# Kernel optimization log

Measured on AMD Instinct MI355X. Metric: run time of the kernel, lower is better.

The kernel has to match this reference:

```python
import jax, jax.numpy as jnp
import numpy as np

B, T, S, V, D, H = 32, 50, 40, 32000, 512, 1024


def setup_inputs() -> dict:
    key = jax.random.key(0)
    ks = jax.random.split(key, 14)
    s_ih = 1.0 / np.sqrt(H)
    return {
        "zh_gruths": jax.random.randint(ks[0], (B, T), 0, V),
        "encoder_hs": jax.random.normal(ks[1], (B, S, H), jnp.float32),
        "encoder_h_n": jax.random.normal(ks[2], (1, B, H), jnp.float32) * 0.1,
        "encoder_c_n": jax.random.normal(ks[3], (1, B, H), jnp.float32) * 0.1,
        "entext_len": jax.random.randint(ks[4], (B,), 1, S + 1),
        "teacher_forcing_ratio": 1,
        "emb": jax.random.normal(ks[5], (V, D), jnp.float32) * 0.02,
        "W_ih": jax.random.normal(ks[6], (4 * H, D), jnp.float32) * s_ih,
        "W_hh": jax.random.normal(ks[7], (4 * H, H), jnp.float32) * s_ih,
        "b_ih": jax.random.normal(ks[8], (4 * H,), jnp.float32) * s_ih,
        "b_hh": jax.random.normal(ks[9], (4 * H,), jnp.float32) * s_ih,
        "W_ht": jax.random.normal(ks[10], (H, 2 * H), jnp.float32) * (1.0 / np.sqrt(2 * H)),
        "b_ht": jnp.zeros((H,), jnp.float32),
        "W_voc": jax.random.normal(ks[11], (V, H), jnp.float32) * s_ih,
        "b_voc": jnp.zeros((V,), jnp.float32),
    }


def reference(zh_gruths, encoder_hs, encoder_h_n, encoder_c_n, entext_len,
              teacher_forcing_ratio, emb, W_ih, W_hh, b_ih, b_hh,
              W_ht, b_ht, W_voc, b_voc):
    # teacher_forcing_ratio == 1 -> always teacher forcing (deterministic branch)
    xs = jnp.swapaxes(emb[zh_gruths], 0, 1)  # [T, B, D]
    hx0, cx0 = encoder_h_n[0], encoder_c_n[0]  # [B, H]

    def step(carry, xt):
        hx, cx = carry
        gates = xt @ W_ih.T + b_ih + hx @ W_hh.T + b_hh  # [B, 4H]
        i, f, g, o = jnp.split(gates, 4, axis=-1)  # torch gate order i,f,g,o
        i, f, o = jax.nn.sigmoid(i), jax.nn.sigmoid(f), jax.nn.sigmoid(o)
        cx = f * cx + i * jnp.tanh(g)
        hx = o * jnp.tanh(cx)
        # dot attention over encoder states
        scores = jnp.einsum('bsh,bh->bs', encoder_hs, hx)
        attn = jax.nn.softmax(scores, axis=-1)
        ctx = jnp.einsum('bs,bsh->bh', attn, encoder_hs)
        hx_atten = jnp.tanh(jnp.concatenate([ctx, hx], axis=-1) @ W_ht.T + b_ht)
        logits_t = hx_atten @ W_voc.T + b_voc  # [B, V]
        return (hx, cx), logits_t

    _, logits = jax.lax.scan(step, (hx0, cx0), xs)  # [T, B, V]
    logits = jnp.swapaxes(logits, 0, 1)  # [B, T, V]
    predicts = jnp.argmax(logits, axis=-1)  # [B, T]
    return logits, predicts
```

## Files before the change

kernel.cpp:

```cpp
#include <hip/hip_runtime.h>
#include <math.h>

typedef short bf16x8 __attribute__((ext_vector_type(8)));
typedef float f32x4 __attribute__((ext_vector_type(4)));
typedef float f32x2 __attribute__((ext_vector_type(2)));
typedef unsigned int uint;
typedef uint u32x4 __attribute__((ext_vector_type(4)));
typedef unsigned long long ull;
typedef unsigned short ushort;

#define Bz 32
#define Tz 50
#define Sz 40
#define Vz 32000
#define Dz 512
#define Hz 1024
#define Mz 1600
#define Mp 1664

__device__ __forceinline__ float bf2f(ushort h) {
    uint u = ((uint)h) << 16;
    return __builtin_bit_cast(float, u);
}
__device__ __forceinline__ void splitf(float f, ushort& hi, ushort& lo) {
    uint u = __builtin_bit_cast(uint, f);
    hi = (ushort)(u >> 16);
    float rem = f - __builtin_bit_cast(float, u & 0xFFFF0000u);
    lo = (ushort)(__builtin_bit_cast(uint, rem) >> 16);
}
__device__ __forceinline__ float sigf(float x) { return 1.f / (1.f + expf(-x)); }

__device__ __forceinline__ uint ld_sc1(const uint* p) {
    uint v;
    asm volatile("global_load_dword %0, %1, off sc0 sc1\n\ts_waitcnt vmcnt(0)"
                 : "=&v"(v) : "v"(p) : "memory");
    return v;
}
__device__ __forceinline__ void st_sc1(uint* p, uint v) {
    asm volatile("global_store_dword %0, %1, off sc0 sc1" :: "v"(p), "v"(v) : "memory");
}

__global__ __launch_bounds__(256) void k_pre(ushort* hxA_hi, ushort* hxA_lo, float* cx,
                                             ushort* AH_hi, ushort* AH_lo, uint* flags,
                                             const float* h0, const float* c0) {
    int gid = blockIdx.x * 256 + threadIdx.x;
    if (gid < 32768) {
        float v = h0[gid];
        ushort hi, lo;
        splitf(v, hi, lo);
        hxA_hi[gid] = hi;
        hxA_lo[gid] = lo;
    } else if (gid < 65536) {
        cx[gid - 32768] = c0[gid - 32768];
    } else if (gid < 196608) {
        int g = gid - 65536;
        AH_hi[(long)Mz * 2048 + g] = 0;
        AH_lo[(long)Mz * 2048 + g] = 0;
    } else if (gid < 196608 + 2048) {
        st_sc1(&flags[gid - 196608], 0u);
    }
}

__global__ __launch_bounds__(256) void k_wsplit(const float* __restrict__ src,
                                                ushort* __restrict__ hi, ushort* __restrict__ lo,
                                                int n4) {
    int stride = gridDim.x * 256;
    for (int i = blockIdx.x * 256 + threadIdx.x; i < n4; i += stride) {
        float4 f = *(const float4*)(src + (long)i * 4);
        float vv[4] = {f.x, f.y, f.z, f.w};
        ushort h[4], l[4];
#pragma unroll
        for (int e = 0; e < 4; ++e) splitf(vv[e], h[e], l[e]);
        uint2 hp, lp;
        hp.x = (uint)h[0] | ((uint)h[1] << 16);
        hp.y = (uint)h[2] | ((uint)h[3] << 16);
        lp.x = (uint)l[0] | ((uint)l[1] << 16);
        lp.y = (uint)l[2] | ((uint)l[3] << 16);
        *(uint2*)(hi + (long)i * 4) = hp;
        *(uint2*)(lo + (long)i * 4) = lp;
    }
}

__global__ __launch_bounds__(256, 1) void k_xgemm(const float* __restrict__ emb,
                                                  const int* __restrict__ tok,
                                                  const float* __restrict__ Wih,
                                                  const float* __restrict__ bih,
                                                  const float* __restrict__ bhh,
                                                  float* __restrict__ gx) {
    __shared__ ushort sAh[128][40];
    __shared__ ushort sAl[128][40];
    __shared__ ushort sBh[128][40];
    __shared__ ushort sBl[128][40];
    int bid = blockIdx.x;
    int mt = bid >> 5, nt = bid & 31;
    int tid = threadIdx.x;
    int row = tid >> 1, half = tid & 1;
    int wv = tid >> 6, lane = tid & 63;
    int wr = wv >> 1, wc = wv & 1;
    int m0 = wr * 64, n0 = wc * 64;
    int r16 = lane & 15, kg = lane >> 4, k0 = kg * 8;

    f32x4 acc[4][4];
#pragma unroll
    for (int i = 0; i < 4; i++)
#pragma unroll
        for (int j = 0; j < 4; j++) acc[i][j] = (f32x4){0.f, 0.f, 0.f, 0.f};

    int r = mt * 128 + row;
    int tk = (r < Mz) ? tok[r] : 0;
    const float* arow = emb + (long)tk * Dz;
    const float* brow = Wih + (long)(nt * 128 + row) * Dz;

    for (int kb = 0; kb < Dz; kb += 32) {
        {
            ushort hh[16], ll[16];
#pragma unroll
            for (int q = 0; q < 16; q += 4) {
                float4 w4 = (r < Mz) ? *(const float4*)(arow + kb + half * 16 + q)
                                     : (float4){0.f, 0.f, 0.f, 0.f};
                float vv[4] = {w4.x, w4.y, w4.z, w4.w};
#pragma unroll
                for (int e = 0; e < 4; ++e) splitf(vv[e], hh[q + e], ll[q + e]);
            }
            *(uint4*)&sAh[row][half * 16]     = *(uint4*)&hh[0];
            *(uint4*)&sAh[row][half * 16 + 8] = *(uint4*)&hh[8];
            *(uint4*)&sAl[row][half * 16]     = *(uint4*)&ll[0];
            *(uint4*)&sAl[row][half * 16 + 8] = *(uint4*)&ll[8];
        }
        {
            ushort hh[16], ll[16];
#pragma unroll
            for (int q = 0; q < 16; q += 4) {
                float4 w4 = *(const float4*)(brow + kb + half * 16 + q);
                float vv[4] = {w4.x, w4.y, w4.z, w4.w};
#pragma unroll
                for (int e = 0; e < 4; ++e) splitf(vv[e], hh[q + e], ll[q + e]);
            }
            *(uint4*)&sBh[row][half * 16]     = *(uint4*)&hh[0];
            *(uint4*)&sBh[row][half * 16 + 8] = *(uint4*)&hh[8];
            *(uint4*)&sBl[row][half * 16]     = *(uint4*)&ll[0];
            *(uint4*)&sBl[row][half * 16 + 8] = *(uint4*)&ll[8];
        }
        __syncthreads();
        bf16x8 af[4], alf[4], bhf[4], blf[4];
#pragma unroll
        for (int i = 0; i < 4; ++i) {
            af[i]  = *(const bf16x8*)&sAh[m0 + i * 16 + r16][k0];
            alf[i] = *(const bf16x8*)&sAl[m0 + i * 16 + r16][k0];
            bhf[i] = *(const bf16x8*)&sBh[n0 + i * 16 + r16][k0];
            blf[i] = *(const bf16x8*)&sBl[n0 + i * 16 + r16][k0];
        }
#pragma unroll
        for (int i = 0; i < 4; ++i)
#pragma unroll
            for (int jn = 0; jn < 4; ++jn) {
                acc[i][jn] = __builtin_amdgcn_mfma_f32_16x16x32_bf16(af[i],  bhf[jn], acc[i][jn], 0, 0, 0);
                acc[i][jn] = __builtin_amdgcn_mfma_f32_16x16x32_bf16(af[i],  blf[jn], acc[i][jn], 0, 0, 0);
                acc[i][jn] = __builtin_amdgcn_mfma_f32_16x16x32_bf16(alf[i], bhf[jn], acc[i][jn], 0, 0, 0);
            }
        __syncthreads();
    }
#pragma unroll
    for (int i = 0; i < 4; ++i) {
        int gr0 = mt * 128 + m0 + i * 16 + kg * 4;
#pragma unroll
        for (int reg = 0; reg < 4; ++reg) {
            int gr = gr0 + reg;
            if (gr >= Mz) continue;
#pragma unroll
            for (int jn = 0; jn < 4; ++jn) {
                int gc = nt * 128 + n0 + jn * 16 + r16;
                gx[(long)gr * 4096 + gc] = acc[i][jn][reg] + bih[gc] + bhh[gc];
            }
        }
    }
}

__global__ __launch_bounds__(512, 1) void k_recfused5(
    const float* __restrict__ gx,
    const ushort* __restrict__ Whi, const ushort* __restrict__ Wlo,
    ushort* __restrict__ hxA_hi, ushort* __restrict__ hxA_lo,
    float* __restrict__ hxh, float* __restrict__ cx,
    const float* __restrict__ enc,
    ushort* __restrict__ AH_hi, ushort* __restrict__ AH_lo,
    uint* flags,
    const float* __restrict__ Wvoc, ushort* __restrict__ Wvh, ushort* __restrict__ Wvl,
    int do_wsplit) {
    __shared__ u32x4 stg4[8192];
    __shared__ float hxs[Hz];
    __shared__ float sc[64];
    __shared__ float aw[64];
    int wid = blockIdx.x, tid = threadIdx.x;

    if (wid >= 96) {
        if (do_wsplit) {
            int n4 = Vz * Hz / 4;
            int stride = 160 * 512;
            for (int i = (wid - 96) * 512 + tid; i < n4; i += stride) {
                float4 f = *(const float4*)(Wvoc + (long)i * 4);
                float vv[4] = {f.x, f.y, f.z, f.w};
                ushort h[4], l[4];
#pragma unroll
                for (int e = 0; e < 4; ++e) splitf(vv[e], h[e], l[e]);
                uint2 hp, lp;
                hp.x = (uint)h[0] | ((uint)h[1] << 16);
                hp.y = (uint)h[2] | ((uint)h[3] << 16);
                lp.x = (uint)l[0] | ((uint)l[1] << 16);
                lp.y = (uint)l[2] | ((uint)l[3] << 16);
                *(uint2*)(Wvh + (long)i * 4) = hp;
                *(uint2*)(Wvl + (long)i * 4) = lp;
            }
        }
        return;
    }

    int lane = tid & 63, kh = tid >> 6;

    for (int t = 0; t <= Tz; ++t) {
        if (wid < 64) {
            if (t < Tz) {
                int w = wid;
                int p = t & 1, q = p ^ 1;
                {
                    bool done = false;
                    while (!done) {
                        uint f = 0xFFFFFFFFu;
                        if (lane < 8) f = ld_sc1(&flags[(kh * 8 + lane) * 16]);
                        done = (bool)__all(f >= (uint)t);
                        if (!done) __builtin_amdgcn_s_sleep(1);
                    }
                }
                int kslot = kh * 16 + (lane & 15);
                int rowb = (lane >> 4) * 8;
                const ushort* ph = hxA_hi + p * 32768 + (long)rowb * 1024 + kslot * 8;
                const ushort* pl = hxA_lo + p * 32768 + (long)rowb * 1024 + kslot * 8;
                {
                    u32x4 d0, d1, d2, d3, d4, d5, d6, d7;
                    asm volatile(
                        "global_load_dwordx4 %0, %8, off sc0 sc1\n\t"
                        "global_load_dwordx4 %1, %9, off sc0 sc1\n\t"
                        "global_load_dwordx4 %2, %10, off sc0 sc1\n\t"
                        "global_load_dwordx4 %3, %11, off sc0 sc1\n\t"
                        "global_load_dwordx4 %4, %12, off sc0 sc1\n\t"
                        "global_load_dwordx4 %5, %13, off sc0 sc1\n\t"
                        "global_load_dwordx4 %6, %14, off sc0 sc1\n\t"
                        "global_load_dwordx4 %7, %15, off sc0 sc1\n\t"
                        "s_waitcnt vmcnt(0)"
                        : "=&v"(d0), "=&v"(d1), "=&v"(d2), "=&v"(d3),
                          "=&v"(d4), "=&v"(d5), "=&v"(d6), "=&v"(d7)
                        : "v"(ph), "v"(ph + 1024), "v"(ph + 2048), "v"(ph + 3072),
                          "v"(ph + 4096), "v"(ph + 5120), "v"(ph + 6144), "v"(ph + 7168)
                        : "memory");
                    int li = kslot * 32;
                    stg4[li + ((rowb + 0 + kslot) & 31)] = d0;
                    stg4[li + ((rowb + 1 + kslot) & 31)] = d1;
                    stg4[li + ((rowb + 2 + kslot) & 31)] = d2;
                    stg4[li + ((rowb + 3 + kslot) & 31)] = d3;
                    stg4[li + ((rowb + 4 + kslot) & 31)] = d4;
                    stg4[li + ((rowb + 5 + kslot) & 31)] = d5;
                    stg4[li + ((rowb + 6 + kslot) & 31)] = d6;
                    stg4[li + ((rowb + 7 + kslot) & 31)] = d7;
                }
                {
                    u32x4 d0, d1, d2, d3, d4, d5, d6, d7;
                    asm volatile(
                        "global_load_dwordx4 %0, %8, off sc0 sc1\n\t"
                        "global_load_dwordx4 %1, %9, off sc0 sc1\n\t"
                        "global_load_dwordx4 %2, %10, off sc0 sc1\n\t"
                        "global_load_dwordx4 %3, %11, off sc0 sc1\n\t"
                        "global_load_dwordx4 %4, %12, off sc0 sc1\n\t"
                        "global_load_dwordx4 %5, %13, off sc0 sc1\n\t"
                        "global_load_dwordx4 %6, %14, off sc0 sc1\n\t"
                        "global_load_dwordx4 %7, %15, off sc0 sc1\n\t"
                        "s_waitcnt vmcnt(0)"
                        : "=&v"(d0), "=&v"(d1), "=&v"(d2), "=&v"(d3),
                          "=&v"(d4), "=&v"(d5), "=&v"(d6), "=&v"(d7)
                        : "v"(pl), "v"(pl + 1024), "v"(pl + 2048), "v"(pl + 3072),
                          "v"(pl + 4096), "v"(pl + 5120), "v"(pl + 6144), "v"(pl + 7168)
                        : "memory");
                    int li = 4096 + kslot * 32;
                    stg4[li + ((rowb + 0 + kslot) & 31)] = d0;
                    stg4[li + ((rowb + 1 + kslot) & 31)] = d1;
                    stg4[li + ((rowb + 2 + kslot) & 31)] = d2;
                    stg4[li + ((rowb + 3 + kslot) & 31)] = d3;
                    stg4[li + ((rowb + 4 + kslot) & 31)] = d4;
                    stg4[li + ((rowb + 5 + kslot) & 31)] = d5;
                    stg4[li + ((rowb + 6 + kslot) & 31)] = d6;
                    stg4[li + ((rowb + 7 + kslot) & 31)] = d7;
                }
                int r16 = lane & 15, kg = lane >> 4;
                int jbase = w * 16 + r16;
                const ushort* whbase = Whi + (long)jbase * 1024;
                const ushort* wlbase = Wlo + (long)jbase * 1024;
                f32x4 acc[2][4];
#pragma unroll
                for (int i = 0; i < 2; ++i)
#pragma unroll
                    for (int v = 0; v < 4; ++v) acc[i][v] = (f32x4){0.f, 0.f, 0.f, 0.f};
#pragma unroll
                for (int it = 0; it < 4; ++it) {
                    int ksl = kh * 16 + it * 4 + kg;
                    int k0 = ksl * 8;
                    bf16x8 a_h0 = *(const bf16x8*)&stg4[       ksl * 32 + ((r16 + ksl) & 31)];
                    bf16x8 a_l0 = *(const bf16x8*)&stg4[4096 + ksl * 32 + ((r16 + ksl) & 31)];
                    bf16x8 a_h1 = *(const bf16x8*)&stg4[       ksl * 32 + ((16 + r16 + ksl) & 31)];
                    bf16x8 a_l1 = *(const bf16x8*)&stg4[4096 + ksl * 32 + ((16 + r16 + ksl) & 31)];
                    bf16x8 bh[4], bl[4];
#pragma unroll
                    for (int v = 0; v < 4; ++v) {
                        bh[v] = *(const bf16x8*)(whbase + ((long)v << 20) + k0);
                        bl[v] = *(const bf16x8*)(wlbase + ((long)v << 20) + k0);
                    }
#pragma unroll
                    for (int v = 0; v < 4; ++v) {
                        acc[0][v] = __builtin_amdgcn_mfma_f32_16x16x32_bf16(a_h0, bh[v], acc[0][v], 0, 0, 0);
                        acc[0][v] = __builtin_amdgcn_mfma_f32_16x16x32_bf16(a_l0, bh[v], acc[0][v], 0, 0, 0);
                        acc[0][v] = __builtin_amdgcn_mfma_f32_16x16x32_bf16(a_h0, bl[v], acc[0][v], 0, 0, 0);
                        acc[1][v] = __builtin_amdgcn_mfma_f32_16x16x32_bf16(a_h1, bh[v], acc[1][v], 0, 0, 0);
                        acc[1][v] = __builtin_amdgcn_mfma_f32_16x16x32_bf16(a_l1, bh[v], acc[1][v], 0, 0, 0);
                        acc[1][v] = __builtin_amdgcn_mfma_f32_16x16x32_bf16(a_h1, bl[v], acc[1][v], 0, 0, 0);
                    }
                }
                __syncthreads();
                float* sgp = (float*)stg4;
#pragma unroll
                for (int i = 0; i < 2; ++i)
#pragma unroll
                    for (int v = 0; v < 4; ++v)
#pragma unroll
                        for (int reg = 0; reg < 4; ++reg)
                            sgp[(((kh * 4 + v) * 32) + i * 16 + kg * 4 + reg) * 16 + r16] = acc[i][v][reg];
                __syncthreads();
                int b = tid >> 4, h16 = tid & 15;
                int hg = w * 16 + h16;
                const float* gxr = gx + ((long)b * Tz + t) * 4096 + hg;
                float g0 = 0.f, g1 = 0.f, g2 = 0.f, g3 = 0.f;
#pragma unroll
                for (int khh = 0; khh < 8; ++khh) {
                    g0 += sgp[((khh * 4 + 0) * 32 + b) * 16 + h16];
                    g1 += sgp[((khh * 4 + 1) * 32 + b) * 16 + h16];
                    g2 += sgp[((khh * 4 + 2) * 32 + b) * 16 + h16];
                    g3 += sgp[((khh * 4 + 3) * 32 + b) * 16 + h16];
                }
                g0 += gxr[0]; g1 += gxr[1024]; g2 += gxr[2048]; g3 += gxr[3072];
                long ci = (long)b * Hz + hg;
                float c = sigf(g1) * cx[ci] + sigf(g0) * tanhf(g2);
                float hv = sigf(g3) * tanhf(c);
                cx[ci] = c;
                float* hp = hxh + ((long)t * Bz + b) * Hz + hg;
                asm volatile("global_store_dword %0, %1, off sc0 sc1" :: "v"(hp), "v"(hv));
                ushort hi, lo;
                splitf(hv, hi, lo);
                ushort* hip = hxA_hi + q * 32768 + ci;
                ushort* lop = hxA_lo + q * 32768 + ci;
                asm volatile("global_store_short %0, %1, off sc0 sc1" :: "v"(hip), "v"((uint)hi));
                asm volatile("global_store_short %0, %1, off sc0 sc1" :: "v"(lop), "v"((uint)lo));
                asm volatile("s_waitcnt vmcnt(0)" ::: "memory");
                __syncthreads();
                if (tid == 0) st_sc1(&flags[wid * 16], (uint)(t + 1));
            }
        } else {
            if (t > 0) {
                int b = wid - 64, tt = t - 1;
                if (tid < 64) {
                    bool done = false;
                    while (!done) {
                        uint f = ld_sc1(&flags[tid * 16]);
                        done = (bool)__all(f >= (uint)t);
                        if (!done) __builtin_amdgcn_s_sleep(2);
                    }
                }
                __syncthreads();
                const float* hsrc = hxh + ((long)tt * Bz + b) * Hz + tid * 2;
                f32x2 h2;
                asm volatile("global_load_dwordx2 %0, %1, off sc0 sc1\n\ts_waitcnt vmcnt(0)"
                             : "=&v"(h2) : "v"(hsrc) : "memory");
                hxs[tid * 2] = h2[0];
                hxs[tid * 2 + 1] = h2[1];
                __syncthreads();
                int wv = tid >> 6;
                float hreg[16];
#pragma unroll
                for (int u = 0; u < 16; ++u) hreg[u] = hxs[lane * 16 + u];
                const float* eb = enc + (long)b * Sz * Hz;
                for (int s = wv; s < Sz; s += 8) {
                    const float* er = eb + (long)s * Hz + lane * 16;
                    float sum = 0.f;
#pragma unroll
                    for (int qq = 0; qq < 4; ++qq) {
                        float4 e4 = *(const float4*)(er + qq * 4);
                        sum += e4.x * hreg[qq*4] + e4.y * hreg[qq*4+1] + e4.z * hreg[qq*4+2] + e4.w * hreg[qq*4+3];
                    }
#pragma unroll
                    for (int off = 32; off >= 1; off >>= 1) sum += __shfl_xor(sum, off);
                    if (lane == 0) sc[s] = sum;
                }
                __syncthreads();
                if (tid < 64) {
                    float vv = (tid < Sz) ? sc[tid] : -3.402823e38f;
                    float mx = vv;
#pragma unroll
                    for (int off = 32; off >= 1; off >>= 1) mx = fmaxf(mx, __shfl_xor(mx, off));
                    float e = (tid < Sz) ? expf(vv - mx) : 0.f;
                    float ssum = e;
#pragma unroll
                    for (int off = 32; off >= 1; off >>= 1) ssum += __shfl_xor(ssum, off);
                    if (tid < Sz) aw[tid] = e / ssum;
                }
                __syncthreads();
                float c0 = 0.f, c1 = 0.f;
#pragma unroll 4
                for (int s = 0; s < Sz; ++s) {
                    float2 e2 = *(const float2*)(eb + (long)s * Hz + tid * 2);
                    float a = aw[s];
                    c0 += a * e2.x; c1 += a * e2.y;
                }
                long rr = (long)b * Tz + tt;
                ushort* dh = AH_hi + rr * 2048;
                ushort* dl = AH_lo + rr * 2048;
                ushort hi, lo;
                splitf(c0, hi, lo); dh[tid * 2]     = hi; dl[tid * 2]     = lo;
                splitf(c1, hi, lo); dh[tid * 2 + 1] = hi; dl[tid * 2 + 1] = lo;
                splitf(hxs[tid * 2],     hi, lo); dh[1024 + tid * 2]     = hi; dl[1024 + tid * 2]     = lo;
                splitf(hxs[tid * 2 + 1], hi, lo); dh[1024 + tid * 2 + 1] = hi; dl[1024 + tid * 2 + 1] = lo;
            }
        }
    }
}

__global__ __launch_bounds__(256, 1) void k_ht(const ushort* __restrict__ Ah,
                                               const ushort* __restrict__ Al,
                                               const ushort* __restrict__ Bh,
                                               const ushort* __restrict__ Bl,
                                               const float* __restrict__ bht,
                                               ushort* __restrict__ Hh, ushort* __restrict__ Hl) {
    __shared__ ushort sAh[128][40];
    __shared__ ushort sAl[128][40];
    __shared__ ushort sBh[128][40];
    __shared__ ushort sBl[128][40];
    int bid = blockIdx.x;
    int mt = bid >> 3, nt = bid & 7;
    int tid = threadIdx.x;
    int row = tid >> 1, half = tid & 1;
    int wv = tid >> 6, lane = tid & 63;
    int wr = wv >> 1, wc = wv & 1;
    int m0 = wr * 64, n0 = wc * 64;
    int r16 = lane & 15, kg = lane >> 4, k0 = kg * 8;

    f32x4 acc[4][4];
#pragma unroll
    for (int i = 0; i < 4; i++)
#pragma unroll
        for (int j = 0; j < 4; j++) acc[i][j] = (f32x4){0.f, 0.f, 0.f, 0.f};

    long arow = (long)(mt * 128 + row) * 2048;
    long brow = (long)(nt * 128 + row) * 2048;

    for (int kb = 0; kb < 2048; kb += 32) {
        const ushort* pa = Ah + arow + kb + half * 16;
        *(uint4*)&sAh[row][half * 16]     = *(const uint4*)pa;
        *(uint4*)&sAh[row][half * 16 + 8] = *(const uint4*)(pa + 8);
        const ushort* pl = Al + arow + kb + half * 16;
        *(uint4*)&sAl[row][half * 16]     = *(const uint4*)pl;
        *(uint4*)&sAl[row][half * 16 + 8] = *(const uint4*)(pl + 8);
        const ushort* pb = Bh + brow + kb + half * 16;
        *(uint4*)&sBh[row][half * 16]     = *(const uint4*)pb;
        *(uint4*)&sBh[row][half * 16 + 8] = *(const uint4*)(pb + 8);
        const ushort* pc = Bl + brow + kb + half * 16;
        *(uint4*)&sBl[row][half * 16]     = *(const uint4*)pc;
        *(uint4*)&sBl[row][half * 16 + 8] = *(const uint4*)(pc + 8);
        __syncthreads();
        bf16x8 af[4], alf[4], bhf[4], blf[4];
#pragma unroll
        for (int i = 0; i < 4; ++i) {
            af[i]  = *(const bf16x8*)&sAh[m0 + i * 16 + r16][k0];
            alf[i] = *(const bf16x8*)&sAl[m0 + i * 16 + r16][k0];
            bhf[i] = *(const bf16x8*)&sBh[n0 + i * 16 + r16][k0];
            blf[i] = *(const bf16x8*)&sBl[n0 + i * 16 + r16][k0];
        }
#pragma unroll
        for (int i = 0; i < 4; ++i)
#pragma unroll
            for (int jn = 0; jn < 4; ++jn) {
                acc[i][jn] = __builtin_amdgcn_mfma_f32_16x16x32_bf16(af[i],  bhf[jn], acc[i][jn], 0, 0, 0);
                acc[i][jn] = __builtin_amdgcn_mfma_f32_16x16x32_bf16(af[i],  blf[jn], acc[i][jn], 0, 0, 0);
                acc[i][jn] = __builtin_amdgcn_mfma_f32_16x16x32_bf16(alf[i], bhf[jn], acc[i][jn], 0, 0, 0);
            }
        __syncthreads();
    }
#pragma unroll
    for (int i = 0; i < 4; ++i) {
        int gr0 = mt * 128 + m0 + i * 16 + kg * 4;
#pragma unroll
        for (int reg = 0; reg < 4; ++reg) {
            int gr = gr0 + reg;
            bool valid = gr < Mz;
#pragma unroll
            for (int jn = 0; jn < 4; ++jn) {
                int gc = nt * 128 + n0 + jn * 16 + r16;
                float vv = tanhf(acc[i][jn][reg] + bht[gc]);
                ushort hi = 0, lo = 0;
                if (valid) splitf(vv, hi, lo);
                Hh[(long)gr * Hz + gc] = hi;
                Hl[(long)gr * Hz + gc] = lo;
            }
        }
    }
}

__global__ __launch_bounds__(256, 1) void k_voc3(
    const ushort* __restrict__ Ah, const ushort* __restrict__ Al,
    const ushort* __restrict__ Wh, const ushort* __restrict__ Wl,
    const float* __restrict__ bvoc,
    float* __restrict__ out, ull* __restrict__ keys) {
    __shared__ ushort sAh[128][40];
    __shared__ ushort sAl[128][40];
    __shared__ ushort sBh[128][40];
    __shared__ ushort sBl[128][40];
    int bid = blockIdx.x;
    int nt = bid % 250, mg = bid / 250;
    int mt_beg = (mg == 0) ? 0 : 7;
    int mt_end = (mg == 0) ? 7 : 13;
    int tid = threadIdx.x;
    int row = tid >> 1, half = tid & 1;
    int wv = tid >> 6, lane = tid & 63;
    int wr = wv >> 1, wc = wv & 1;
    int m0 = wr * 64, n0 = wc * 64;
    int r16 = lane & 15, kg = lane >> 4, k0 = kg * 8;

    long wrow = (long)(nt * 128 + row) * Hz;
    int vcol_base = nt * 128 + n0;

    for (int mt = mt_beg; mt < mt_end; ++mt) {
        f32x4 acc[4][4];
#pragma unroll
        for (int i = 0; i < 4; i++)
#pragma unroll
            for (int j = 0; j < 4; j++) acc[i][j] = (f32x4){0.f, 0.f, 0.f, 0.f};

        long arow = (long)(mt * 128 + row) * Hz;

        for (int kb = 0; kb < Hz; kb += 32) {
            const ushort* pa = Ah + arow + kb + half * 16;
            *(uint4*)&sAh[row][half * 16]     = *(const uint4*)pa;
            *(uint4*)&sAh[row][half * 16 + 8] = *(const uint4*)(pa + 8);
            const ushort* pl = Al + arow + kb + half * 16;
            *(uint4*)&sAl[row][half * 16]     = *(const uint4*)pl;
            *(uint4*)&sAl[row][half * 16 + 8] = *(const uint4*)(pl + 8);
            const ushort* pb = Wh + wrow + kb + half * 16;
            *(uint4*)&sBh[row][half * 16]     = *(const uint4*)pb;
            *(uint4*)&sBh[row][half * 16 + 8] = *(const uint4*)(pb + 8);
            const ushort* pc = Wl + wrow + kb + half * 16;
            *(uint4*)&sBl[row][half * 16]     = *(const uint4*)pc;
            *(uint4*)&sBl[row][half * 16 + 8] = *(const uint4*)(pc + 8);
            __syncthreads();
            bf16x8 af[4], alf[4], bhf[4], blf[4];
#pragma unroll
            for (int i = 0; i < 4; ++i) {
                af[i]  = *(const bf16x8*)&sAh[m0 + i * 16 + r16][k0];
                alf[i] = *(const bf16x8*)&sAl[m0 + i * 16 + r16][k0];
                bhf[i] = *(const bf16x8*)&sBh[n0 + i * 16 + r16][k0];
                blf[i] = *(const bf16x8*)&sBl[n0 + i * 16 + r16][k0];
            }
#pragma unroll
            for (int i = 0; i < 4; ++i)
#pragma unroll
                for (int jn = 0; jn < 4; ++jn) {
                    acc[i][jn] = __builtin_amdgcn_mfma_f32_16x16x32_bf16(af[i],  bhf[jn], acc[i][jn], 0, 0, 0);
                    acc[i][jn] = __builtin_amdgcn_mfma_f32_16x16x32_bf16(af[i],  blf[jn], acc[i][jn], 0, 0, 0);
                    acc[i][jn] = __builtin_amdgcn_mfma_f32_16x16x32_bf16(alf[i], bhf[jn], acc[i][jn], 0, 0, 0);
                }
            __syncthreads();
        }
#pragma unroll
        for (int i = 0; i < 4; ++i) {
            int gr0 = mt * 128 + m0 + i * 16 + kg * 4;
#pragma unroll
            for (int reg = 0; reg < 4; ++reg) {
                int gr = gr0 + reg;
                bool valid = gr < Mz;
                float bestv = -3.402823e38f;
                int bestc = 0;
#pragma unroll
                for (int jn = 0; jn < 4; ++jn) {
                    int gc = vcol_base + jn * 16 + r16;
                    float v = acc[i][jn][reg] + bvoc[gc];
                    if (valid) __builtin_nontemporal_store(v, &out[(long)gr * Vz + gc]);
                    if (v > bestv) { bestv = v; bestc = gc; }
                }
#pragma unroll
                for (int off = 1; off < 16; off <<= 1) {
                    float ov = __shfl_xor(bestv, off);
                    int oc = __shfl_xor(bestc, off);
                    if (ov > bestv || (ov == bestv && oc < bestc)) { bestv = ov; bestc = oc; }
                }
                if (valid && r16 == 0) {
                    uint u = __builtin_bit_cast(uint, bestv);
                    u = (u & 0x80000000u) ? ~u : (u | 0x80000000u);
                    keys[(long)gr * 512 + nt * 2 + wc] = (((ull)u) << 32) | (ull)(65535 - bestc);
                }
            }
        }
    }
}

__global__ __launch_bounds__(256) void k_argmax2(const ull* __restrict__ keys, float* __restrict__ pred) {
    int r = blockIdx.x, tid = threadIdx.x;
    ull best = 0;
    for (int j = tid; j < 500; j += 256) {
        ull k = keys[(long)r * 512 + j];
        if (k > best) best = k;
    }
    __shared__ ull sk[256];
    sk[tid] = best;
    __syncthreads();
    for (int s = 128; s > 0; s >>= 1) {
        if (tid < s) { if (sk[tid + s] > sk[tid]) sk[tid] = sk[tid + s]; }
        __syncthreads();
    }
    if (tid == 0) pred[r] = (float)(65535 - (int)(sk[0] & 0xFFFFull));
}

extern "C" void kernel_launch(void* const* d_in, const int* in_sizes, int n_in,
                              void* d_out, int out_size, void* d_ws, size_t ws_size,
                              hipStream_t stream) {
    const int*   tok  = (const int*)d_in[0];
    const float* enc  = (const float*)d_in[1];
    const float* h0   = (const float*)d_in[2];
    const float* c0   = (const float*)d_in[3];
    const float* emb  = (const float*)d_in[6];
    const float* Wih  = (const float*)d_in[7];
    const float* Whh  = (const float*)d_in[8];
    const float* bih  = (const float*)d_in[9];
    const float* bhh  = (const float*)d_in[10];
    const float* Wht  = (const float*)d_in[11];
    const float* bht  = (const float*)d_in[12];
    const float* Wvoc = (const float*)d_in[13];
    const float* bvoc = (const float*)d_in[14];
    float* out = (float*)d_out;

    char* base = (char*)d_ws;
    size_t off = 0;
    float*  gx      = (float*)(base + off);  off += (size_t)Mz * 4096 * 4;
    ushort* hxA_hi  = (ushort*)(base + off); off += 2 * 32768 * 2;
    ushort* hxA_lo  = (ushort*)(base + off); off += 2 * 32768 * 2;
    float*  cx      = (float*)(base + off);  off += 32768 * 4;
    float*  hxh     = (float*)(base + off);  off += (size_t)Tz * Bz * Hz * 4;
    ushort* AH_hi   = (ushort*)(base + off); off += (size_t)Mp * 2048 * 2;
    ushort* AH_lo   = (ushort*)(base + off); off += (size_t)Mp * 2048 * 2;
    ushort* Whh_hi  = (ushort*)(base + off); off += (size_t)4096 * 1024 * 2;
    ushort* Whh_lo  = (ushort*)(base + off); off += (size_t)4096 * 1024 * 2;
    ushort* Wht_hi  = (ushort*)(base + off); off += (size_t)1024 * 2048 * 2;
    ushort* Wht_lo  = (ushort*)(base + off); off += (size_t)1024 * 2048 * 2;

    const size_t wvoc_bytes = (size_t)Vz * Hz * 2 * 2;
    const size_t surv_bytes = (size_t)Mp * 1024 * 2 * 2 + (size_t)Mz * 512 * 8 + 8192;
    bool fused = ws_size >= off + wvoc_bytes + surv_bytes;

    ushort* Wvoc_hi; ushort* Wvoc_lo; size_t off2;
    if (fused) {
        Wvoc_hi = (ushort*)(base + off);
        Wvoc_lo = Wvoc_hi + (size_t)Vz * Hz;
        off2 = off + wvoc_bytes;
    } else {
        Wvoc_hi = (ushort*)base;
        Wvoc_lo = Wvoc_hi + (size_t)Vz * Hz;
        off2 = wvoc_bytes;
    }
    ushort* HXA_hi  = (ushort*)(base + off2); off2 += (size_t)Mp * 1024 * 2;
    ushort* HXA_lo  = (ushort*)(base + off2); off2 += (size_t)Mp * 1024 * 2;
    ull*    keys    = (ull*)(base + off2);    off2 += (size_t)Mz * 512 * 8;
    uint*   flags   = (uint*)(base + off2);   off2 += 8192;

    k_pre<<<776, 256, 0, stream>>>(hxA_hi, hxA_lo, cx, AH_hi, AH_lo, flags, h0, c0);
    k_wsplit<<<1024, 256, 0, stream>>>(Whh, Whh_hi, Whh_lo, 4096 * 1024 / 4);
    k_wsplit<<<512, 256, 0, stream>>>(Wht, Wht_hi, Wht_lo, 1024 * 2048 / 4);
    k_xgemm<<<13 * 32, 256, 0, stream>>>(emb, tok, Wih, bih, bhh, gx);

    k_recfused5<<<fused ? 256 : 96, 512, 0, stream>>>(
        gx, Whh_hi, Whh_lo, hxA_hi, hxA_lo, hxh, cx, enc, AH_hi, AH_lo, flags,
        Wvoc, Wvoc_hi, Wvoc_lo, fused ? 1 : 0);

    k_ht<<<13 * 8, 256, 0, stream>>>(AH_hi, AH_lo, Wht_hi, Wht_lo, bht, HXA_hi, HXA_lo);
    if (!fused) {
        k_wsplit<<<2048, 256, 0, stream>>>(Wvoc, Wvoc_hi, Wvoc_lo, Vz * Hz / 4);
    }
    k_voc3<<<500, 256, 0, stream>>>(HXA_hi, HXA_lo, Wvoc_hi, Wvoc_lo, bvoc, out, keys);
    k_argmax2<<<Mz, 256, 0, stream>>>(keys, out + (long)Mz * Vz);
}
```

Baseline: 1.136 ms.

## Compute vocab GEMM in single bf16 and fix argmax with fp32 candidate rescan

The vocabulary projection drops from a three-MFMA bf16x3 split to one bf16 MFMA. Only the rounded high half of W_voc is converted and stored, and the activation is split with round-to-nearest. The fp32 logits written to the output now carry bf16-level error. A new rescan kernel recomputes in fp32 the candidates that lie within a norm-based margin of each row's max, so the predicted argmax stays exact. This cuts GEMM MFMA work and W_voc traffic, but adds a per-row scan and dot-product pass and lowers the accuracy of the logits themselves.

```diff
diff --git a/kernel.cpp b/kernel.cpp
--- a/kernel.cpp
+++ b/kernel.cpp
@@ -17,7 +17,12 @@
 #define Hz 1024
 #define Mz 1600
 #define Mp 1664
-
+#define CAP 1024
+
+__device__ __forceinline__ ushort f2bf(float f) {
+    uint u = __builtin_bit_cast(uint, f);
+    return (ushort)((u + 0x7FFFu + ((u >> 16) & 1u)) >> 16);
+}
 __device__ __forceinline__ float bf2f(ushort h) {
     uint u = ((uint)h) << 16;
     return __builtin_bit_cast(float, u);
@@ -27,6 +32,10 @@
     hi = (ushort)(u >> 16);
     float rem = f - __builtin_bit_cast(float, u & 0xFFFF0000u);
     lo = (ushort)(__builtin_bit_cast(uint, rem) >> 16);
+}
+__device__ __forceinline__ void splitrn(float f, ushort& hi, ushort& lo) {
+    hi = f2bf(f);
+    lo = f2bf(f - bf2f(hi));
 }
 __device__ __forceinline__ float sigf(float x) { return 1.f / (1.f + expf(-x)); }
 
@@ -81,6 +90,18 @@
     }
 }
 
+__global__ __launch_bounds__(256) void k_wbf16(const float* __restrict__ src,
+                                               ushort* __restrict__ dst, int n4) {
+    int stride = gridDim.x * 256;
+    for (int i = blockIdx.x * 256 + threadIdx.x; i < n4; i += stride) {
+        float4 f = *(const float4*)(src + (long)i * 4);
+        uint2 hp;
+        hp.x = (uint)f2bf(f.x) | ((uint)f2bf(f.y) << 16);
+        hp.y = (uint)f2bf(f.z) | ((uint)f2bf(f.w) << 16);
+        *(uint2*)(dst + (long)i * 4) = hp;
+    }
+}
+
 __global__ __launch_bounds__(256, 1) void k_xgemm(const float* __restrict__ emb,
                                                   const int* __restrict__ tok,
                                                   const float* __restrict__ Wih,
@@ -176,7 +197,7 @@
     }
 }
 
-__global__ __launch_bounds__(512, 1) void k_recfused5(
+__global__ __launch_bounds__(512, 1) void k_recfused7(
     const float* __restrict__ gx,
     const ushort* __restrict__ Whi, const ushort* __restrict__ Wlo,
     ushort* __restrict__ hxA_hi, ushort* __restrict__ hxA_lo,
@@ -184,7 +205,7 @@
     const float* __restrict__ enc,
     ushort* __restrict__ AH_hi, ushort* __restrict__ AH_lo,
     uint* flags,
-    const float* __restrict__ Wvoc, ushort* __restrict__ Wvh, ushort* __restrict__ Wvl,
+    const float* __restrict__ Wvoc, ushort* __restrict__ Wvh,
     int do_wsplit) {
     __shared__ u32x4 stg4[8192];
     __shared__ float hxs[Hz];
@@ -198,17 +219,10 @@
             int stride = 160 * 512;
             for (int i = (wid - 96) * 512 + tid; i < n4; i += stride) {
                 float4 f = *(const float4*)(Wvoc + (long)i * 4);
-                float vv[4] = {f.x, f.y, f.z, f.w};
-                ushort h[4], l[4];
-#pragma unroll
-                for (int e = 0; e < 4; ++e) splitf(vv[e], h[e], l[e]);
-                uint2 hp, lp;
-                hp.x = (uint)h[0] | ((uint)h[1] << 16);
-                hp.y = (uint)h[2] | ((uint)h[3] << 16);
-                lp.x = (uint)l[0] | ((uint)l[1] << 16);
-                lp.y = (uint)l[2] | ((uint)l[3] << 16);
+                uint2 hp;
+                hp.x = (uint)f2bf(f.x) | ((uint)f2bf(f.y) << 16);
+                hp.y = (uint)f2bf(f.z) | ((uint)f2bf(f.w) << 16);
                 *(uint2*)(Wvh + (long)i * 4) = hp;
-                *(uint2*)(Wvl + (long)i * 4) = lp;
             }
         }
         return;
@@ -232,9 +246,10 @@
                 }
                 int kslot = kh * 16 + (lane & 15);
                 int rowb = (lane >> 4) * 8;
-                const ushort* ph = hxA_hi + p * 32768 + (long)rowb * 1024 + kslot * 8;
-                const ushort* pl = hxA_lo + p * 32768 + (long)rowb * 1024 + kslot * 8;
-                {
+                const ushort* planes[2] = { hxA_hi + p * 32768, hxA_lo + p * 32768 };
+#pragma unroll
+                for (int plane = 0; plane < 2; ++plane) {
+                    const ushort* b0 = planes[plane] + (long)rowb * 1024 + kslot * 8;
                     u32x4 d0, d1, d2, d3, d4, d5, d6, d7;
                     asm volatile(
                         "global_load_dwordx4 %0, %8, off sc0 sc1\n\t"
@@ -248,37 +263,10 @@
                         "s_waitcnt vmcnt(0)"
                         : "=&v"(d0), "=&v"(d1), "=&v"(d2), "=&v"(d3),
                           "=&v"(d4), "=&v"(d5), "=&v"(d6), "=&v"(d7)
-                        : "v"(ph), "v"(ph + 1024), "v"(ph + 2048), "v"(ph + 3072),
-                          "v"(ph + 4096), "v"(ph + 5120), "v"(ph + 6144), "v"(ph + 7168)
+                        : "v"(b0), "v"(b0 + 1024), "v"(b0 + 2048), "v"(b0 + 3072),
+                          "v"(b0 + 4096), "v"(b0 + 5120), "v"(b0 + 6144), "v"(b0 + 7168)
                         : "memory");
-                    int li = kslot * 32;
-                    stg4[li + ((rowb + 0 + kslot) & 31)] = d0;
-                    stg4[li + ((rowb + 1 + kslot) & 31)] = d1;
-                    stg4[li + ((rowb + 2 + kslot) & 31)] = d2;
-                    stg4[li + ((rowb + 3 + kslot) & 31)] = d3;
-                    stg4[li + ((rowb + 4 + kslot) & 31)] = d4;
-                    stg4[li + ((rowb + 5 + kslot) & 31)] = d5;
-                    stg4[li + ((rowb + 6 + kslot) & 31)] = d6;
-                    stg4[li + ((rowb + 7 + kslot) & 31)] = d7;
-                }
-                {
-                    u32x4 d0, d1, d2, d3, d4, d5, d6, d7;
-                    asm volatile(
-                        "global_load_dwordx4 %0, %8, off sc0 sc1\n\t"
-                        "global_load_dwordx4 %1, %9, off sc0 sc1\n\t"
-                        "global_load_dwordx4 %2, %10, off sc0 sc1\n\t"
-                        "global_load_dwordx4 %3, %11, off sc0 sc1\n\t"
-                        "global_load_dwordx4 %4, %12, off sc0 sc1\n\t"
-                        "global_load_dwordx4 %5, %13, off sc0 sc1\n\t"
-                        "global_load_dwordx4 %6, %14, off sc0 sc1\n\t"
-                        "global_load_dwordx4 %7, %15, off sc0 sc1\n\t"
-                        "s_waitcnt vmcnt(0)"
-                        : "=&v"(d0), "=&v"(d1), "=&v"(d2), "=&v"(d3),
-                          "=&v"(d4), "=&v"(d5), "=&v"(d6), "=&v"(d7)
-                        : "v"(pl), "v"(pl + 1024), "v"(pl + 2048), "v"(pl + 3072),
-                          "v"(pl + 4096), "v"(pl + 5120), "v"(pl + 6144), "v"(pl + 7168)
-                        : "memory");
-                    int li = 4096 + kslot * 32;
+                    int li = plane * 4096 + kslot * 32;
                     stg4[li + ((rowb + 0 + kslot) & 31)] = d0;
                     stg4[li + ((rowb + 1 + kslot) & 31)] = d1;
                     stg4[li + ((rowb + 2 + kslot) & 31)] = d2;
@@ -500,7 +488,7 @@
                 int gc = nt * 128 + n0 + jn * 16 + r16;
                 float vv = tanhf(acc[i][jn][reg] + bht[gc]);
                 ushort hi = 0, lo = 0;
-                if (valid) splitf(vv, hi, lo);
+                if (valid) splitrn(vv, hi, lo);
                 Hh[(long)gr * Hz + gc] = hi;
                 Hl[(long)gr * Hz + gc] = lo;
             }
@@ -508,15 +496,12 @@
     }
 }
 
-__global__ __launch_bounds__(256, 1) void k_voc3(
-    const ushort* __restrict__ Ah, const ushort* __restrict__ Al,
-    const ushort* __restrict__ Wh, const ushort* __restrict__ Wl,
+__global__ __launch_bounds__(256, 2) void k_voc4(
+    const ushort* __restrict__ Ah, const ushort* __restrict__ Wh,
     const float* __restrict__ bvoc,
     float* __restrict__ out, ull* __restrict__ keys) {
     __shared__ ushort sAh[128][40];
-    __shared__ ushort sAl[128][40];
     __shared__ ushort sBh[128][40];
-    __shared__ ushort sBl[128][40];
     int bid = blockIdx.x;
     int nt = bid % 250, mg = bid / 250;
     int mt_beg = (mg == 0) ? 0 : 7;
@@ -544,32 +529,21 @@
             const ushort* pa = Ah + arow + kb + half * 16;
             *(uint4*)&sAh[row][half * 16]     = *(const uint4*)pa;
             *(uint4*)&sAh[row][half * 16 + 8] = *(const uint4*)(pa + 8);
-            const ushort* pl = Al + arow + kb + half * 16;
-            *(uint4*)&sAl[row][half * 16]     = *(const uint4*)pl;
-            *(uint4*)&sAl[row][half * 16 + 8] = *(const uint4*)(pl + 8);
             const ushort* pb = Wh + wrow + kb + half * 16;
             *(uint4*)&sBh[row][half * 16]     = *(const uint4*)pb;
             *(uint4*)&sBh[row][half * 16 + 8] = *(const uint4*)(pb + 8);
-            const ushort* pc = Wl + wrow + kb + half * 16;
-            *(uint4*)&sBl[row][half * 16]     = *(const uint4*)pc;
-            *(uint4*)&sBl[row][half * 16 + 8] = *(const uint4*)(pc + 8);
             __syncthreads();
-            bf16x8 af[4], alf[4], bhf[4], blf[4];
+            bf16x8 af[4], bhf[4];
 #pragma unroll
             for (int i = 0; i < 4; ++i) {
                 af[i]  = *(const bf16x8*)&sAh[m0 + i * 16 + r16][k0];
-                alf[i] = *(const bf16x8*)&sAl[m0 + i * 16 + r16][k0];
                 bhf[i] = *(const bf16x8*)&sBh[n0 + i * 16 + r16][k0];
-                blf[i] = *(const bf16x8*)&sBl[n0 + i * 16 + r16][k0];
             }
 #pragma unroll
             for (int i = 0; i < 4; ++i)
 #pragma unroll
-                for (int jn = 0; jn < 4; ++jn) {
-                    acc[i][jn] = __builtin_amdgcn_mfma_f32_16x16x32_bf16(af[i],  bhf[jn], acc[i][jn], 0, 0, 0);
-                    acc[i][jn] = __builtin_amdgcn_mfma_f32_16x16x32_bf16(af[i],  blf[jn], acc[i][jn], 0, 0, 0);
-                    acc[i][jn] = __builtin_amdgcn_mfma_f32_16x16x32_bf16(alf[i], bhf[jn], acc[i][jn], 0, 0, 0);
-                }
+                for (int jn = 0; jn < 4; ++jn)
+                    acc[i][jn] = __builtin_amdgcn_mfma_f32_16x16x32_bf16(af[i], bhf[jn], acc[i][jn], 0, 0, 0);
             __syncthreads();
         }
 #pragma unroll
@@ -604,7 +578,8 @@
     }
 }
 
-__global__ __launch_bounds__(256) void k_argmax2(const ull* __restrict__ keys, float* __restrict__ pred) {
+__global__ __launch_bounds__(256) void k_argmax3(const ull* __restrict__ keys,
+                                                 float* __restrict__ amax) {
     int r = blockIdx.x, tid = threadIdx.x;
     ull best = 0;
     for (int j = tid; j < 500; j += 256) {
@@ -618,7 +593,100 @@
         if (tid < s) { if (sk[tid + s] > sk[tid]) sk[tid] = sk[tid + s]; }
         __syncthreads();
     }
-    if (tid == 0) pred[r] = (float)(65535 - (int)(sk[0] & 0xFFFFull));
+    if (tid == 0) {
+        uint e = (uint)(sk[0] >> 32);
+        uint orig = (e & 0x80000000u) ? (e & 0x7FFFFFFFu) : ~e;
+        amax[r] = __builtin_bit_cast(float, orig);
+    }
+}
+
+__global__ __launch_bounds__(256) void k_rescan(
+    const float* __restrict__ out, const float* __restrict__ amax,
+    const ushort* __restrict__ Ah, const ushort* __restrict__ Al,
+    const float* __restrict__ Wvoc, const float* __restrict__ bvoc,
+    float* __restrict__ pred) {
+    int r = blockIdx.x, tid = threadIdx.x;
+    __shared__ float arow[Hz];
+    __shared__ int cand[CAP];
+    __shared__ int ccnt;
+    __shared__ float cval[4];
+    __shared__ float sv[256];
+    __shared__ int   si[256];
+    if (tid == 0) ccnt = 0;
+    float sq = 0.f;
+#pragma unroll
+    for (int u = 0; u < 4; ++u) {
+        int j = tid + 256 * u;
+        float a = bf2f(Ah[(long)r * Hz + j]) + bf2f(Al[(long)r * Hz + j]);
+        arow[j] = a;
+        sq += a * a;
+    }
+#pragma unroll
+    for (int off = 32; off >= 1; off >>= 1) sq += __shfl_xor(sq, off);
+    if ((tid & 63) == 0) cval[tid >> 6] = sq;
+    __syncthreads();
+    float nrm = sqrtf((cval[0] + cval[1]) + (cval[2] + cval[3]));
+    float margin = 0.0094f * nrm + 0.01f;
+    float thr = amax[r] - margin;
+    __syncthreads();
+    const float* rowp = out + (long)r * Vz;
+    for (int c = tid; c < Vz; c += 256) {
+        float v = rowp[c];
+        if (v >= thr) {
+            int slot = atomicAdd(&ccnt, 1);
+            if (slot < CAP) cand[slot] = c;
+        }
+    }
+    __syncthreads();
+    int n = ccnt;
+    int besti;
+    if (n <= CAP) {
+        float bestv = -3.402823e38f;
+        besti = 0x7FFFFFFF;
+        for (int k = 0; k < n; ++k) {
+            int c = cand[k];
+            const float* wr = Wvoc + (long)c * Hz;
+            float s = 0.f;
+#pragma unroll
+            for (int u = 0; u < 4; ++u) {
+                int j = tid + 256 * u;
+                s += arow[j] * wr[j];
+            }
+#pragma unroll
+            for (int off = 32; off >= 1; off >>= 1) s += __shfl_xor(s, off);
+            if ((tid & 63) == 0) cval[tid >> 6] = s;
+            __syncthreads();
+            float tot = (cval[0] + cval[1]) + (cval[2] + cval[3]) + bvoc[c];
+            if (tot > bestv || (tot == bestv && c < besti)) { bestv = tot; besti = c; }
+            __syncthreads();
+        }
+    } else {
+        float bv = -3.402823e38f;
+        int bi = 0x7FFFFFFF;
+        for (int c = tid; c < Vz; c += 256) {
+            const float* wr = Wvoc + (long)c * Hz;
+            float s = 0.f;
+            for (int j = 0; j < Hz; j += 4) {
+                float4 w4 = *(const float4*)(wr + j);
+                s += arow[j] * w4.x + arow[j + 1] * w4.y + arow[j + 2] * w4.z + arow[j + 3] * w4.w;
+            }
+            s += bvoc[c];
+            if (s > bv || (s == bv && c < bi)) { bv = s; bi = c; }
+        }
+        sv[tid] = bv; si[tid] = bi;
+        __syncthreads();
+        for (int s2 = 128; s2 > 0; s2 >>= 1) {
+            if (tid < s2) {
+                if (sv[tid + s2] > sv[tid] ||
+                    (sv[tid + s2] == sv[tid] && si[tid + s2] < si[tid])) {
+                    sv[tid] = sv[tid + s2]; si[tid] = si[tid + s2];
+                }
+            }
+            __syncthreads();
+        }
+        besti = si[0];
+    }
+    if (tid == 0) pred[r] = (float)besti;
 }
 
 extern "C" void kernel_launch(void* const* d_in, const int* in_sizes, int n_in,
@@ -653,23 +721,22 @@
     ushort* Wht_hi  = (ushort*)(base + off); off += (size_t)1024 * 2048 * 2;
     ushort* Wht_lo  = (ushort*)(base + off); off += (size_t)1024 * 2048 * 2;
 
-    const size_t wvoc_bytes = (size_t)Vz * Hz * 2 * 2;
-    const size_t surv_bytes = (size_t)Mp * 1024 * 2 * 2 + (size_t)Mz * 512 * 8 + 8192;
-    bool fused = ws_size >= off + wvoc_bytes + surv_bytes;
-
-    ushort* Wvoc_hi; ushort* Wvoc_lo; size_t off2;
+    const size_t wvh_bytes  = (size_t)Vz * Hz * 2;
+    const size_t surv_bytes = (size_t)Mp * 1024 * 2 * 2 + (size_t)Mz * 512 * 8 + 8192 + 8192;
+    bool fused = ws_size >= off + wvh_bytes + surv_bytes;
+
+    ushort* Wvh; size_t off2;
     if (fused) {
-        Wvoc_hi = (ushort*)(base + off);
-        Wvoc_lo = Wvoc_hi + (size_t)Vz * Hz;
-        off2 = off + wvoc_bytes;
+        Wvh = (ushort*)(base + off);
+        off2 = off + wvh_bytes;
     } else {
-        Wvoc_hi = (ushort*)base;
-        Wvoc_lo = Wvoc_hi + (size_t)Vz * Hz;
-        off2 = wvoc_bytes;
+        Wvh = (ushort*)base;
+        off2 = wvh_bytes;
     }
     ushort* HXA_hi  = (ushort*)(base + off2); off2 += (size_t)Mp * 1024 * 2;
     ushort* HXA_lo  = (ushort*)(base + off2); off2 += (size_t)Mp * 1024 * 2;
     ull*    keys    = (ull*)(base + off2);    off2 += (size_t)Mz * 512 * 8;
+    float*  amax    = (float*)(base + off2);  off2 += 8192;
     uint*   flags   = (uint*)(base + off2);   off2 += 8192;
 
     k_pre<<<776, 256, 0, stream>>>(hxA_hi, hxA_lo, cx, AH_hi, AH_lo, flags, h0, c0);
@@ -677,14 +744,16 @@
     k_wsplit<<<512, 256, 0, stream>>>(Wht, Wht_hi, Wht_lo, 1024 * 2048 / 4);
     k_xgemm<<<13 * 32, 256, 0, stream>>>(emb, tok, Wih, bih, bhh, gx);
 
-    k_recfused5<<<fused ? 256 : 96, 512, 0, stream>>>(
+    k_recfused7<<<fused ? 256 : 96, 512, 0, stream>>>(
         gx, Whh_hi, Whh_lo, hxA_hi, hxA_lo, hxh, cx, enc, AH_hi, AH_lo, flags,
-        Wvoc, Wvoc_hi, Wvoc_lo, fused ? 1 : 0);
+        Wvoc, Wvh, fused ? 1 : 0);
 
     k_ht<<<13 * 8, 256, 0, stream>>>(AH_hi, AH_lo, Wht_hi, Wht_lo, bht, HXA_hi, HXA_lo);
     if (!fused) {
-        k_wsplit<<<2048, 256, 0, stream>>>(Wvoc, Wvoc_hi, Wvoc_lo, Vz * Hz / 4);
-    }
-    k_voc3<<<500, 256, 0, stream>>>(HXA_hi, HXA_lo, Wvoc_hi, Wvoc_lo, bvoc, out, keys);
-    k_argmax2<<<Mz, 256, 0, stream>>>(keys, out + (long)Mz * Vz);
-}
+        k_wbf16<<<2048, 256, 0, stream>>>(Wvoc, Wvh, Vz * Hz / 4);
+    }
+    k_voc4<<<500, 256, 0, stream>>>(HXA_hi, Wvh, bvoc, out, keys);
+    k_argmax3<<<Mz, 256, 0, stream>>>(keys, amax);
+    k_rescan<<<Mz, 256, 0, stream>>>(out, amax, HXA_hi, HXA_lo, Wvoc, bvoc,
+                                     out + (long)Mz * Vz);
+}
```

Result: faster. 1.073 ms (-5.6%).
